# Kernel tuning notes

Measured on AMD Instinct MI355X. Metric: run time of the kernel, lower is better.

The kernel has to match this reference:

```python
import jax, jax.numpy as jnp
import numpy as np

EPS = 1e-5


def gcn_conv(x, src, dst, n_nodes, W, b):
    # x: [B, N, Fin]; src/dst: [E+N] (self loops included); W: [Fout, Fin]
    h = jnp.einsum('bnf,of->bno', x, W)                      # [B, N, Fout]
    deg = jnp.zeros((n_nodes,), h.dtype).at[dst].add(1.0)    # in-degree of A+I
    dinv = jnp.where(deg > 0, 1.0 / jnp.sqrt(deg), 0.0)
    norm = dinv[src] * dinv[dst]                             # [E+N]
    msg = h[:, src, :] * norm[None, :, None]                 # gather along node axis
    out = jnp.zeros_like(h).at[:, dst, :].add(msg)           # scatter-add aggregate
    return out + b


def batchnorm_nodes(x, gamma, beta):
    # torch BatchNorm1d(N) on [B, N, C]: channel axis is N, stats over (B, C)
    mean = jnp.mean(x, axis=(0, 2), keepdims=True)
    var = jnp.mean(jnp.square(x - mean), axis=(0, 2), keepdims=True)
    xn = (x - mean) * jax.lax.rsqrt(var + EPS)
    return xn * gamma[None, :, None] + beta[None, :, None]


def setup_inputs() -> dict:
    key = jax.random.key(0)
    ks = jax.random.split(key, 20)
    B, N, FIN, D, OUT, E = 4096, 64, 67, 2048, 2, 512
    s = 0.1
    d = {}
    d['x_fingerprints'] = jax.random.normal(ks[0], (B, D), jnp.float32)
    d['x_node_features'] = jax.random.normal(ks[1], (B, N, FIN), jnp.float32)
    d['edge_list'] = jax.random.randint(ks[2], (2, E), 0, N)
    d['W1'] = jax.random.normal(ks[3], (64, FIN), jnp.float32) * s
    d['b1'] = jax.random.normal(ks[4], (64,), jnp.float32) * s
    d['g1'] = 1.0 + jax.random.normal(ks[5], (N,), jnp.float32) * s
    d['be1'] = jax.random.normal(ks[6], (N,), jnp.float32) * s
    d['W2'] = jax.random.normal(ks[7], (32, 64), jnp.float32) * s
    d['b2'] = jax.random.normal(ks[8], (32,), jnp.float32) * s
    d['g2'] = 1.0 + jax.random.normal(ks[9], (N,), jnp.float32) * s
    d['be2'] = jax.random.normal(ks[10], (N,), jnp.float32) * s
    d['Wl1'] = jax.random.normal(ks[11], (400, D), jnp.float32) * (s / 4)
    d['bl1'] = jax.random.normal(ks[12], (400,), jnp.float32) * s
    d['Wl2'] = jax.random.normal(ks[13], (64, 400), jnp.float32) * s
    d['bl2'] = jax.random.normal(ks[14], (64,), jnp.float32) * s
    d['Wfc'] = jax.random.normal(ks[15], (OUT, 96), jnp.float32) * s
    d['bfc'] = jax.random.normal(ks[16], (OUT,), jnp.float32) * s
    return d


def reference(x_fingerprints, x_node_features, edge_list, W1, b1, g1, be1,
              W2, b2, g2, be2, Wl1, bl1, Wl2, bl2, Wfc, bfc):
    B, N, _ = x_node_features.shape
    loops = jnp.arange(N)
    src = jnp.concatenate([edge_list[0], loops])  # add self loops (GCNConv default)
    dst = jnp.concatenate([edge_list[1], loops])
    g = gcn_conv(x_node_features, src, dst, N, W1, b1)
    g = jax.nn.relu(batchnorm_nodes(g, g1, be1))
    g = gcn_conv(g, src, dst, N, W2, b2)
    g = jax.nn.relu(batchnorm_nodes(g, g2, be2))           # [B, N, 32]
    pooled = jnp.max(g, axis=1)                             # global_max_pool -> [B, 32]
    h = jax.nn.relu(x_fingerprints @ Wl1.T + bl1)
    h = jax.nn.relu(h @ Wl2.T + bl2)                        # [B, 64]
    out = jnp.concatenate([pooled, h], axis=1) @ Wfc.T + bfc
    return out
```

## Files before the change

### kernel.cpp

```cpp
#include <hip/hip_runtime.h>
#include <hip/hip_bf16.h>
#include <math.h>

typedef __bf16 bf16;
typedef __attribute__((ext_vector_type(8))) __bf16 bf16x8;
typedef __attribute__((ext_vector_type(4))) __bf16 bf16x4;
typedef __attribute__((ext_vector_type(4))) float f32x4;

#define EPSBN 1e-5f
#define B_    4096
#define N_    64
#define FIN_  67
#define E_    512
#define NSLOT 128

__global__ __launch_bounds__(256) void k0_prep(const int* __restrict__ edge,
    const float* __restrict__ W1, const float* __restrict__ W2,
    float* __restrict__ partials,
    bf16* __restrict__ an_hi, bf16* __restrict__ an_lo,
    bf16* __restrict__ wpad,
    bf16* __restrict__ w2pad)
{
    int tid = threadIdx.x;
    for (int i = blockIdx.x * 256 + tid; i < NSLOT * 64 * 4; i += gridDim.x * 256)
        partials[i] = 0.f;
    if (blockIdx.x == 1) {
        for (int i = tid; i < 64 * 104; i += 256) {
            int n = i / 104, f = i % 104;
            wpad[i] = (f < FIN_) ? (bf16)W1[n * FIN_ + f] : (bf16)0.f;
        }
        return;
    }
    if (blockIdx.x == 2) {
        for (int i = tid; i < 32 * 72; i += 256) {
            int o = i / 72, f = i % 72;
            w2pad[i] = (f < 64) ? (bf16)W2[o * 64 + f] : (bf16)0.f;
        }
        return;
    }
    if (blockIdx.x != 0) return;

    __shared__ float An[64 * 64];
    __shared__ int ssrc[E_], sdst[E_];
    __shared__ int deg[N_];
    __shared__ float dinv[N_];
    for (int i = tid; i < 64 * 64; i += 256) An[i] = 0.f;
    for (int i = tid; i < E_; i += 256) { ssrc[i] = edge[i]; sdst[i] = edge[E_ + i]; }
    if (tid < N_) deg[tid] = 1;
    __syncthreads();
    for (int i = tid; i < E_; i += 256) atomicAdd(&deg[sdst[i]], 1);
    __syncthreads();
    if (tid < N_) dinv[tid] = rsqrtf((float)deg[tid]);
    __syncthreads();
    for (int i = tid; i < E_; i += 256) {
        int s = ssrc[i], d = sdst[i];
        atomicAdd(&An[d * 64 + s], dinv[s] * dinv[d]);
    }
    if (tid < N_) atomicAdd(&An[tid * 64 + tid], dinv[tid] * dinv[tid]);
    __syncthreads();
    for (int i = tid; i < 64 * 64; i += 256) {
        float v = An[i];
        bf16 h = (bf16)v;
        an_hi[i] = h;
        an_lo[i] = (bf16)(v - (float)h);
    }
}

__global__ __launch_bounds__(256) void k1_gcn1(
    const float* __restrict__ x,
    const float* __restrict__ b1,
    const bf16* __restrict__ an_hi, const bf16* __restrict__ an_lo,
    const bf16* __restrict__ wpad,
    bf16* __restrict__ g1out,
    float* __restrict__ part1)
{
    __shared__ union {
        struct { float xraw[4352]; bf16 wb[64 * 104]; } s0;
        struct { bf16 hhi[64 * 72]; bf16 hlo[64 * 72]; bf16 ost[64 * 72]; } s1;
    } u;
    int tid = threadIdx.x, b = blockIdx.x;
    int w = tid >> 6, lane = tid & 63, q = lane >> 4, r15 = lane & 15;
    int arow = w * 16 + r15;

    const bf16* ahp = an_hi + arow * 64 + q * 8;
    const bf16* alp = an_lo + arow * 64 + q * 8;
    bf16x8 Ah0 = *(const bf16x8*)ahp;
    bf16x8 Ah1 = *(const bf16x8*)(ahp + 32);
    bf16x8 Al0 = *(const bf16x8*)alp;
    bf16x8 Al1 = *(const bf16x8*)(alp + 32);

    const f32x4* xb4 = (const f32x4*)(x + (size_t)b * (N_ * FIN_));
    f32x4* xl4 = (f32x4*)u.s0.xraw;
    for (int i = tid; i < 1072; i += 256) xl4[i] = xb4[i];
    const bf16x8* wg8 = (const bf16x8*)wpad;
    bf16x8* wl8 = (bf16x8*)u.s0.wb;
    for (int i = tid; i < 832; i += 256) wl8[i] = wg8[i];
    __syncthreads();

    f32x4 z4 = {0.f, 0.f, 0.f, 0.f};
    f32x4 acc[4] = {z4, z4, z4, z4};
    const float* xr = u.s0.xraw + arow * FIN_;
#pragma unroll
    for (int kt = 0; kt < 3; ++kt) {
        bf16x8 a;
        int k0 = kt * 32 + q * 8;
#pragma unroll
        for (int j = 0; j < 8; ++j) {
            int k = k0 + j;
            a[j] = (k < FIN_) ? (bf16)xr[k] : (bf16)0.f;
        }
#pragma unroll
        for (int nt = 0; nt < 4; ++nt) {
            bf16x8 bb = *(const bf16x8*)&u.s0.wb[(nt * 16 + r15) * 104 + k0];
            acc[nt] = __builtin_amdgcn_mfma_f32_16x16x32_bf16(a, bb, acc[nt], 0, 0, 0);
        }
    }
    __syncthreads();

    int sbase = w * 16 + q * 4;
#pragma unroll
    for (int nt = 0; nt < 4; ++nt) {
        int c = nt * 16 + r15;
        bf16x4 hi, lo;
#pragma unroll
        for (int r = 0; r < 4; ++r) {
            float v = acc[nt][r];
            bf16 h = (bf16)v;
            hi[r] = h;
            lo[r] = (bf16)(v - (float)h);
        }
        *(bf16x4*)&u.s1.hhi[c * 72 + sbase] = hi;
        *(bf16x4*)&u.s1.hlo[c * 72 + sbase] = lo;
    }
    __syncthreads();

    f32x4 acc2[4] = {z4, z4, z4, z4};
#pragma unroll
    for (int kt = 0; kt < 2; ++kt) {
        bf16x8 Ahk = kt ? Ah1 : Ah0;
        bf16x8 Alk = kt ? Al1 : Al0;
#pragma unroll
        for (int nt = 0; nt < 4; ++nt) {
            int o = (nt * 16 + r15) * 72 + kt * 32 + q * 8;
            bf16x8 Hh = *(const bf16x8*)&u.s1.hhi[o];
            bf16x8 Hl = *(const bf16x8*)&u.s1.hlo[o];
            acc2[nt] = __builtin_amdgcn_mfma_f32_16x16x32_bf16(Ahk, Hh, acc2[nt], 0, 0, 0);
            acc2[nt] = __builtin_amdgcn_mfma_f32_16x16x32_bf16(Ahk, Hl, acc2[nt], 0, 0, 0);
            acc2[nt] = __builtin_amdgcn_mfma_f32_16x16x32_bf16(Alk, Hh, acc2[nt], 0, 0, 0);
        }
    }

    float rs1[4] = {0.f, 0.f, 0.f, 0.f}, rs2[4] = {0.f, 0.f, 0.f, 0.f};
#pragma unroll
    for (int nt = 0; nt < 4; ++nt) {
        int c = nt * 16 + r15;
        float bc = b1[c];
#pragma unroll
        for (int r = 0; r < 4; ++r) {
            float v = acc2[nt][r] + bc;
            rs1[r] += v; rs2[r] += v * v;
            u.s1.ost[(w * 16 + q * 4 + r) * 72 + c] = (bf16)v;
        }
    }
#pragma unroll
    for (int r = 0; r < 4; ++r)
#pragma unroll
        for (int o = 1; o < 16; o <<= 1) {
            rs1[r] += __shfl_xor(rs1[r], o);
            rs2[r] += __shfl_xor(rs2[r], o);
        }
    if (r15 == 0) {
        int slot = b & (NSLOT - 1);
#pragma unroll
        for (int r = 0; r < 4; ++r) {
            int d = w * 16 + q * 4 + r;
            atomicAdd(&part1[(slot * 64 + d) * 2 + 0], rs1[r]);
            atomicAdd(&part1[(slot * 64 + d) * 2 + 1], rs2[r]);
        }
    }
    __syncthreads();
    int n = tid >> 2, oq = tid & 3;
    bf16x8 o0 = *(const bf16x8*)&u.s1.ost[n * 72 + oq * 16];
    bf16x8 o1 = *(const bf16x8*)&u.s1.ost[n * 72 + oq * 16 + 8];
    bf16* gp = g1out + ((size_t)b * 4096 + n * 64 + oq * 16);
    *(bf16x8*)gp = o0;
    *(bf16x8*)(gp + 8) = o1;
}

__global__ __launch_bounds__(64) void k_bnstats(
    const float* __restrict__ part,
    const float* __restrict__ gamma, const float* __restrict__ beta,
    float* __restrict__ scale, float* __restrict__ shift, float inv_count)
{
    int n = blockIdx.x, t = threadIdx.x;
    float s1 = part[(t * 64 + n) * 2] + part[((t + 64) * 64 + n) * 2];
    float s2 = part[(t * 64 + n) * 2 + 1] + part[((t + 64) * 64 + n) * 2 + 1];
#pragma unroll
    for (int o = 32; o > 0; o >>= 1) { s1 += __shfl_down(s1, o); s2 += __shfl_down(s2, o); }
    if (t == 0) {
        float mean = s1 * inv_count;
        float var = s2 * inv_count - mean * mean;
        float sc = gamma[n] * rsqrtf(var + EPSBN);
        scale[n] = sc;
        shift[n] = beta[n] - mean * sc;
    }
}

__global__ __launch_bounds__(256) void k3_gcn2(
    const bf16* __restrict__ g1out,
    const float* __restrict__ b2,
    const float* __restrict__ scale1, const float* __restrict__ shift1,
    const bf16* __restrict__ an_hi, const bf16* __restrict__ an_lo,
    const bf16* __restrict__ w2pad,
    bf16* __restrict__ g2out,
    float* __restrict__ part2)
{
    __shared__ union {
        struct { bf16 graw[4096]; bf16 wb[32 * 72]; } s0;
        struct { bf16 hhi[32 * 72]; bf16 hlo[32 * 72]; bf16 ost[64 * 40]; } s1;
    } u;
    int tid = threadIdx.x, b = blockIdx.x;
    int w = tid >> 6, lane = tid & 63, q = lane >> 4, r15 = lane & 15;
    int arow = w * 16 + r15;

    const bf16* ahp = an_hi + arow * 64 + q * 8;
    const bf16* alp = an_lo + arow * 64 + q * 8;
    bf16x8 Ah0 = *(const bf16x8*)ahp;
    bf16x8 Ah1 = *(const bf16x8*)(ahp + 32);
    bf16x8 Al0 = *(const bf16x8*)alp;
    bf16x8 Al1 = *(const bf16x8*)(alp + 32);
    float sc = scale1[arow], sh = shift1[arow];

    const bf16x8* gg8 = (const bf16x8*)(g1out + (size_t)b * 4096);
    bf16x8* gl8 = (bf16x8*)u.s0.graw;
    for (int i = tid; i < 512; i += 256) gl8[i] = gg8[i];
    const bf16x8* wg8 = (const bf16x8*)w2pad;
    bf16x8* wl8 = (bf16x8*)u.s0.wb;
    for (int i = tid; i < 288; i += 256) wl8[i] = wg8[i];
    __syncthreads();

    f32x4 z4 = {0.f, 0.f, 0.f, 0.f};
    f32x4 acc[2] = {z4, z4};
#pragma unroll
    for (int kt = 0; kt < 2; ++kt) {
        int k0 = kt * 32 + q * 8;
        bf16x8 raw = *(const bf16x8*)&u.s0.graw[arow * 64 + k0];
        bf16x8 a;
#pragma unroll
        for (int j = 0; j < 8; ++j)
            a[j] = (bf16)fmaxf(fmaf(sc, (float)raw[j], sh), 0.f);
#pragma unroll
        for (int nt = 0; nt < 2; ++nt) {
            bf16x8 bb = *(const bf16x8*)&u.s0.wb[(nt * 16 + r15) * 72 + k0];
            acc[nt] = __builtin_amdgcn_mfma_f32_16x16x32_bf16(a, bb, acc[nt], 0, 0, 0);
        }
    }
    __syncthreads();

    int sbase = w * 16 + q * 4;
#pragma unroll
    for (int nt = 0; nt < 2; ++nt) {
        int c = nt * 16 + r15;
        bf16x4 hi, lo;
#pragma unroll
        for (int r = 0; r < 4; ++r) {
            float v = acc[nt][r];
            bf16 h = (bf16)v;
            hi[r] = h;
            lo[r] = (bf16)(v - (float)h);
        }
        *(bf16x4*)&u.s1.hhi[c * 72 + sbase] = hi;
        *(bf16x4*)&u.s1.hlo[c * 72 + sbase] = lo;
    }
    __syncthreads();

    f32x4 acc2[2] = {z4, z4};
#pragma unroll
    for (int kt = 0; kt < 2; ++kt) {
        bf16x8 Ahk = kt ? Ah1 : Ah0;
        bf16x8 Alk = kt ? Al1 : Al0;
#pragma unroll
        for (int nt = 0; nt < 2; ++nt) {
            int o = (nt * 16 + r15) * 72 + kt * 32 + q * 8;
            bf16x8 Hh = *(const bf16x8*)&u.s1.hhi[o];
            bf16x8 Hl = *(const bf16x8*)&u.s1.hlo[o];
            acc2[nt] = __builtin_amdgcn_mfma_f32_16x16x32_bf16(Ahk, Hh, acc2[nt], 0, 0, 0);
            acc2[nt] = __builtin_amdgcn_mfma_f32_16x16x32_bf16(Ahk, Hl, acc2[nt], 0, 0, 0);
            acc2[nt] = __builtin_amdgcn_mfma_f32_16x16x32_bf16(Alk, Hh, acc2[nt], 0, 0, 0);
        }
    }

    float rs1[4] = {0.f, 0.f, 0.f, 0.f}, rs2[4] = {0.f, 0.f, 0.f, 0.f};
#pragma unroll
    for (int nt = 0; nt < 2; ++nt) {
        int c = nt * 16 + r15;
        float bc = b2[c];
#pragma unroll
        for (int r = 0; r < 4; ++r) {
            float v = acc2[nt][r] + bc;
            rs1[r] += v; rs2[r] += v * v;
            u.s1.ost[(w * 16 + q * 4 + r) * 40 + c] = (bf16)v;
        }
    }
#pragma unroll
    for (int r = 0; r < 4; ++r)
#pragma unroll
        for (int o = 1; o < 16; o <<= 1) {
            rs1[r] += __shfl_xor(rs1[r], o);
            rs2[r] += __shfl_xor(rs2[r], o);
        }
    if (r15 == 0) {
        int slot = b & (NSLOT - 1);
#pragma unroll
        for (int r = 0; r < 4; ++r) {
            int d = w * 16 + q * 4 + r;
            atomicAdd(&part2[(slot * 64 + d) * 2 + 0], rs1[r]);
            atomicAdd(&part2[(slot * 64 + d) * 2 + 1], rs2[r]);
        }
    }
    __syncthreads();
    int n = tid >> 2, oq = tid & 3;
    bf16x8 ov = *(const bf16x8*)&u.s1.ost[n * 40 + oq * 8];
    *(bf16x8*)(g2out + ((size_t)b * 2048 + n * 32 + oq * 8)) = ov;
}

__global__ __launch_bounds__(256) void k6_mlp1(
    const float* __restrict__ A,
    const float* __restrict__ Bw,
    float* __restrict__ part)
{
    __shared__ bf16 As[64 * 36];
    __shared__ bf16 Bs[64 * 36];
    int tid = threadIdx.x;
    int m0 = blockIdx.x * 64, n0 = blockIdx.y * 64, ks = blockIdx.z;
    int row = tid >> 2, seg = tid & 3;
    int w = tid >> 6, lane = tid & 63, q = lane >> 4, r15 = lane & 15;
    f32x4 z4 = {0.f, 0.f, 0.f, 0.f};
    f32x4 acc[4] = {z4, z4, z4, z4};
    const float* pA = A + (size_t)(m0 + row) * 2048 + ks * 512 + seg * 8;
    bool bvalid = (n0 + row) < 400;
    const float* pB = Bw + (size_t)(n0 + row) * 2048 + ks * 512 + seg * 8;

    f32x4 a0 = *(const f32x4*)pA;
    f32x4 a1 = *(const f32x4*)(pA + 4);
    f32x4 c0 = z4, c1 = z4;
    if (bvalid) { c0 = *(const f32x4*)pB; c1 = *(const f32x4*)(pB + 4); }

    for (int kt = 0; kt < 16; ++kt) {
        bf16x8 apk, bpk;
        apk[0] = (bf16)a0[0]; apk[1] = (bf16)a0[1]; apk[2] = (bf16)a0[2]; apk[3] = (bf16)a0[3];
        apk[4] = (bf16)a1[0]; apk[5] = (bf16)a1[1]; apk[6] = (bf16)a1[2]; apk[7] = (bf16)a1[3];
        bpk[0] = (bf16)c0[0]; bpk[1] = (bf16)c0[1]; bpk[2] = (bf16)c0[2]; bpk[3] = (bf16)c0[3];
        bpk[4] = (bf16)c1[0]; bpk[5] = (bf16)c1[1]; bpk[6] = (bf16)c1[2]; bpk[7] = (bf16)c1[3];
        __syncthreads();
        *(bf16x8*)&As[row * 36 + seg * 8] = apk;
        *(bf16x8*)&Bs[row * 36 + seg * 8] = bpk;
        __syncthreads();
        if (kt < 15) {
            pA += 32; pB += 32;
            a0 = *(const f32x4*)pA; a1 = *(const f32x4*)(pA + 4);
            if (bvalid) { c0 = *(const f32x4*)pB; c1 = *(const f32x4*)(pB + 4); }
        }
        bf16x8 a = *(const bf16x8*)&As[(w * 16 + r15) * 36 + q * 8];
#pragma unroll
        for (int nt = 0; nt < 4; ++nt) {
            bf16x8 bb = *(const bf16x8*)&Bs[(nt * 16 + r15) * 36 + q * 8];
            acc[nt] = __builtin_amdgcn_mfma_f32_16x16x32_bf16(a, bb, acc[nt], 0, 0, 0);
        }
    }
    float* pp = part + (size_t)ks * 1638400;
#pragma unroll
    for (int nt = 0; nt < 4; ++nt)
#pragma unroll
        for (int r = 0; r < 4; ++r) {
            int mm = m0 + w * 16 + q * 4 + r;
            int nn = n0 + nt * 16 + r15;
            if (nn < 400) pp[(size_t)mm * 400 + nn] = acc[nt][r];
        }
}

__global__ __launch_bounds__(256) void k6_reduce(
    const float* __restrict__ part,
    const float* __restrict__ bias,
    bf16* __restrict__ h1)
{
    int i = blockIdx.x * 256 + threadIdx.x;
    const f32x4* p = (const f32x4*)part;
    f32x4 s0 = p[i], s1v = p[i + 409600], s2v = p[i + 819200], s3v = p[i + 1228800];
    int nn = (i * 4) % 400;
    f32x4 bv = *(const f32x4*)&bias[nn];
    bf16x4 ov;
    ov[0] = (bf16)fmaxf(s0[0] + s1v[0] + s2v[0] + s3v[0] + bv[0], 0.f);
    ov[1] = (bf16)fmaxf(s0[1] + s1v[1] + s2v[1] + s3v[1] + bv[1], 0.f);
    ov[2] = (bf16)fmaxf(s0[2] + s1v[2] + s2v[2] + s3v[2] + bv[2], 0.f);
    ov[3] = (bf16)fmaxf(s0[3] + s1v[3] + s2v[3] + s3v[3] + bv[3], 0.f);
    *(bf16x4*)&h1[i * 4] = ov;
}

__global__ __launch_bounds__(256) void k7_mlp2(
    const bf16* __restrict__ A,
    const float* __restrict__ Bw,
    const float* __restrict__ bias,
    float* __restrict__ Cout)
{
    __shared__ bf16 As[16 * 416];
    int tid = threadIdx.x;
    int m0 = blockIdx.x * 16;
    for (int i = tid; i < 16 * 50; i += 256) {
        int rr = i / 50, cc = (i % 50) * 8;
        *(bf16x8*)&As[rr * 416 + cc] = *(const bf16x8*)(A + (size_t)(m0 + rr) * 400 + cc);
    }
    if (tid < 32) {
        int rr = tid >> 1, cc = 400 + (tid & 1) * 8;
        bf16x8 z;
#pragma unroll
        for (int k = 0; k < 8; ++k) z[k] = (bf16)0.f;
        *(bf16x8*)&As[rr * 416 + cc] = z;
    }
    __syncthreads();

    int w = tid >> 6, lane = tid & 63, q = lane >> 4, r15 = lane & 15;
    f32x4 acc = {0.f, 0.f, 0.f, 0.f};
    const float* pB = Bw + (size_t)(w * 16 + r15) * 400;
#pragma unroll 4
    for (int kt = 0; kt < 13; ++kt) {
        int k0 = kt * 32 + q * 8;
        bf16x8 a = *(const bf16x8*)&As[r15 * 416 + k0];
        bf16x8 bb;
#pragma unroll
        for (int k = 0; k < 8; ++k) bb[k] = (bf16)0.f;
        if (k0 < 400) {
            f32x4 c0 = *(const f32x4*)(pB + k0);
            f32x4 c1 = *(const f32x4*)(pB + k0 + 4);
            bb[0] = (bf16)c0[0]; bb[1] = (bf16)c0[1]; bb[2] = (bf16)c0[2]; bb[3] = (bf16)c0[3];
            bb[4] = (bf16)c1[0]; bb[5] = (bf16)c1[1]; bb[6] = (bf16)c1[2]; bb[7] = (bf16)c1[3];
        }
        acc = __builtin_amdgcn_mfma_f32_16x16x32_bf16(a, bb, acc, 0, 0, 0);
    }
#pragma unroll
    for (int r = 0; r < 4; ++r) {
        int mm = m0 + q * 4 + r;
        int nn = w * 16 + r15;
        float v = fmaxf(acc[r] + bias[nn], 0.f);
        Cout[(size_t)mm * 64 + nn] = v;
    }
}

__global__ __launch_bounds__(256) void k8_final(
    const bf16* __restrict__ g2out,
    const float* __restrict__ scale2, const float* __restrict__ shift2,
    const float* __restrict__ h2,
    const float* __restrict__ Wfc,
    const float* __restrict__ bfc,
    float* __restrict__ out)
{
    __shared__ float s2s[64], sh2s[64];
    int tid = threadIdx.x;
    if (tid < 64) { s2s[tid] = scale2[tid]; sh2s[tid] = shift2[tid]; }
    __syncthreads();
    int w = tid >> 6, lane = tid & 63;
    int b = blockIdx.x * 4 + w;
    int c = lane & 31, half = lane >> 5;
    const bf16* gb = g2out + (size_t)b * 2048;
    float mx = 0.f;
    for (int i = 0; i < 32; ++i) {
        int n = half * 32 + i;
        float v = (float)gb[n * 32 + c];
        float val = fmaf(s2s[n], v, sh2s[n]);
        mx = fmaxf(mx, val);
    }
    mx = fmaxf(mx, __shfl_xor(mx, 32));
    float h2v = h2[(size_t)b * 64 + lane];
#pragma unroll
    for (int o = 0; o < 2; ++o) {
        float t = h2v * Wfc[o * 96 + 32 + lane];
        if (half == 0) t += mx * Wfc[o * 96 + c];
#pragma unroll
        for (int off = 32; off > 0; off >>= 1) t += __shfl_xor(t, off);
        if (lane == 0) out[(size_t)b * 2 + o] = t + bfc[o];
    }
}

extern "C" void kernel_launch(void* const* d_in, const int* in_sizes, int n_in,
                              void* d_out, int out_size, void* d_ws, size_t ws_size,
                              hipStream_t stream)
{
    const float* x_fp   = (const float*)d_in[0];
    const float* x_node = (const float*)d_in[1];
    const int*   edge   = (const int*)d_in[2];
    const float* W1     = (const float*)d_in[3];
    const float* b1     = (const float*)d_in[4];
    const float* g1     = (const float*)d_in[5];
    const float* be1    = (const float*)d_in[6];
    const float* W2     = (const float*)d_in[7];
    const float* b2     = (const float*)d_in[8];
    const float* g2     = (const float*)d_in[9];
    const float* be2    = (const float*)d_in[10];
    const float* Wl1    = (const float*)d_in[11];
    const float* bl1    = (const float*)d_in[12];
    const float* Wl2    = (const float*)d_in[13];
    const float* bl2    = (const float*)d_in[14];
    const float* Wfc    = (const float*)d_in[15];
    const float* bfc    = (const float*)d_in[16];
    float* out = (float*)d_out;

    char* ws = (char*)d_ws;
    float* scale1  = (float*)(ws + 5632);
    float* shift1  = (float*)(ws + 5888);
    float* scale2  = (float*)(ws + 6144);
    float* shift2  = (float*)(ws + 6400);
    float* part1   = (float*)(ws + 8192);
    float* part2   = (float*)(ws + 8192 + 65536);
    bf16*  g1out   = (bf16*)(ws + 139264);
    float* part6   = (float*)(ws + 139264);
    bf16*  g2out   = (bf16*)(ws + 33693696ull);
    bf16*  h1      = (bf16*)(ws + 50470912ull);
    float* h2      = (float*)(ws + 53747712ull);
    bf16*  an_hi   = (bf16*)(ws + 53747712ull);
    bf16*  an_lo   = (bf16*)(ws + 53747712ull + 8192);
    bf16*  wpad    = (bf16*)(ws + 53747712ull + 16384);
    bf16*  w2pad   = (bf16*)(ws + 53747712ull + 32768);

    k0_prep<<<dim3(64), dim3(256), 0, stream>>>(edge, W1, W2, part1, an_hi, an_lo, wpad, w2pad);
    k1_gcn1<<<dim3(4096), dim3(256), 0, stream>>>(x_node, b1, an_hi, an_lo, wpad, g1out, part1);
    k_bnstats<<<dim3(64), dim3(64), 0, stream>>>(part1, g1, be1, scale1, shift1,
                                                 1.f / (4096.f * 64.f));
    k3_gcn2<<<dim3(4096), dim3(256), 0, stream>>>(g1out, b2, scale1, shift1,
                                                  an_hi, an_lo, w2pad, g2out, part2);
    k_bnstats<<<dim3(64), dim3(64), 0, stream>>>(part2, g2, be2, scale2, shift2,
                                                 1.f / (4096.f * 32.f));
    k6_mlp1<<<dim3(64, 7, 4), dim3(256), 0, stream>>>(x_fp, Wl1, part6);
    k6_reduce<<<dim3(1600), dim3(256), 0, stream>>>(part6, bl1, h1);
    k7_mlp2<<<dim3(256), dim3(256), 0, stream>>>(h1, Wl2, bl2, h2);
    k8_final<<<dim3(1024), dim3(256), 0, stream>>>(g2out, scale2, shift2, h2, Wfc, bfc, out);
}
```

Before: 269.0 us.

## Process four graphs per block with register prefetch and register-resident weights

Both GCN kernels now loop over four batch elements per block. Each block keeps its W fragments and bias in registers instead of staging them through shared memory, and loads the next graph's input into registers while the current one is computed. BN partial statistics are now taken from the bf16-rounded outputs after the store, with a short 4-lane shuffle. Launch bounds are tightened to raise occupancy. In exchange the grid is 4x smaller, there are more registers per thread, and the statistics are computed on rounded values.

Result: faster. 241.3 us (-10.3%).

```diff
diff --git a/kernel.cpp b/kernel.cpp
--- a/kernel.cpp
+++ b/kernel.cpp
@@ -66,7 +66,7 @@
     }
 }
 
-__global__ __launch_bounds__(256) void k1_gcn1(
+__global__ __launch_bounds__(256, 3) void k1_gcn1(
     const float* __restrict__ x,
     const float* __restrict__ b1,
     const bf16* __restrict__ an_hi, const bf16* __restrict__ an_lo,
@@ -74,13 +74,21 @@
     bf16* __restrict__ g1out,
     float* __restrict__ part1)
 {
-    __shared__ union {
-        struct { float xraw[4352]; bf16 wb[64 * 104]; } s0;
-        struct { bf16 hhi[64 * 72]; bf16 hlo[64 * 72]; bf16 ost[64 * 72]; } s1;
-    } u;
-    int tid = threadIdx.x, b = blockIdx.x;
+    __shared__ float xraw[4352];
+    __shared__ bf16 hhi[64 * 72];
+    __shared__ bf16 hlo[64 * 72];
+    __shared__ bf16 ost[64 * 72];
+
+    int tid = threadIdx.x;
     int w = tid >> 6, lane = tid & 63, q = lane >> 4, r15 = lane & 15;
     int arow = w * 16 + r15;
+
+    bf16x8 wf[3][4];
+#pragma unroll
+    for (int kt = 0; kt < 3; ++kt)
+#pragma unroll
+        for (int nt = 0; nt < 4; ++nt)
+            wf[kt][nt] = *(const bf16x8*)&wpad[(nt * 16 + r15) * 104 + kt * 32 + q * 8];
 
     const bf16* ahp = an_hi + arow * 64 + q * 8;
     const bf16* alp = an_lo + arow * 64 + q * 8;
@@ -89,102 +97,112 @@
     bf16x8 Al0 = *(const bf16x8*)alp;
     bf16x8 Al1 = *(const bf16x8*)(alp + 32);
 
-    const f32x4* xb4 = (const f32x4*)(x + (size_t)b * (N_ * FIN_));
-    f32x4* xl4 = (f32x4*)u.s0.xraw;
-    for (int i = tid; i < 1072; i += 256) xl4[i] = xb4[i];
-    const bf16x8* wg8 = (const bf16x8*)wpad;
-    bf16x8* wl8 = (bf16x8*)u.s0.wb;
-    for (int i = tid; i < 832; i += 256) wl8[i] = wg8[i];
-    __syncthreads();
-
+    float bc[4];
+#pragma unroll
+    for (int nt = 0; nt < 4; ++nt) bc[nt] = b1[nt * 16 + r15];
+
+    size_t b0 = (size_t)blockIdx.x * 4;
+    const f32x4* xb4 = (const f32x4*)(x + b0 * 4288);
+
+    f32x4 pre0 = xb4[tid], pre1 = xb4[tid + 256], pre2 = xb4[tid + 512], pre3 = xb4[tid + 768];
+    f32x4 pre4 = {0.f, 0.f, 0.f, 0.f};
+    if (tid < 48) pre4 = xb4[tid + 1024];
+
+    f32x4* xl4 = (f32x4*)xraw;
     f32x4 z4 = {0.f, 0.f, 0.f, 0.f};
-    f32x4 acc[4] = {z4, z4, z4, z4};
-    const float* xr = u.s0.xraw + arow * FIN_;
-#pragma unroll
-    for (int kt = 0; kt < 3; ++kt) {
-        bf16x8 a;
-        int k0 = kt * 32 + q * 8;
+
+#pragma unroll 1
+    for (int g = 0; g < 4; ++g) {
+        int b = (int)b0 + g;
+        xl4[tid] = pre0; xl4[tid + 256] = pre1; xl4[tid + 512] = pre2; xl4[tid + 768] = pre3;
+        if (tid < 48) xl4[tid + 1024] = pre4;
+        __syncthreads();
+
+        f32x4 acc[4] = {z4, z4, z4, z4};
+        const float* xr = xraw + arow * FIN_;
+#pragma unroll
+        for (int kt = 0; kt < 3; ++kt) {
+            bf16x8 a;
+            if (kt < 2) {
+                int k0 = kt * 32 + q * 8;
+#pragma unroll
+                for (int j = 0; j < 8; ++j) a[j] = (bf16)xr[k0 + j];
+            } else {
+#pragma unroll
+                for (int j = 0; j < 8; ++j) a[j] = (bf16)0.f;
+                if (q == 0) { a[0] = (bf16)xr[64]; a[1] = (bf16)xr[65]; a[2] = (bf16)xr[66]; }
+            }
+#pragma unroll
+            for (int nt = 0; nt < 4; ++nt)
+                acc[nt] = __builtin_amdgcn_mfma_f32_16x16x32_bf16(a, wf[kt][nt], acc[nt], 0, 0, 0);
+        }
+        if (g < 3) {
+            const f32x4* xn = xb4 + (size_t)(g + 1) * 1072;
+            pre0 = xn[tid]; pre1 = xn[tid + 256]; pre2 = xn[tid + 512]; pre3 = xn[tid + 768];
+            if (tid < 48) pre4 = xn[tid + 1024];
+        }
+        __syncthreads();
+
+        int sbase = w * 16 + q * 4;
+#pragma unroll
+        for (int nt = 0; nt < 4; ++nt) {
+            int c = nt * 16 + r15;
+            bf16x4 hi, lo;
+#pragma unroll
+            for (int r = 0; r < 4; ++r) {
+                float v = acc[nt][r];
+                bf16 h = (bf16)v;
+                hi[r] = h; lo[r] = (bf16)(v - (float)h);
+            }
+            *(bf16x4*)&hhi[c * 72 + sbase] = hi;
+            *(bf16x4*)&hlo[c * 72 + sbase] = lo;
+        }
+        __syncthreads();
+
+        f32x4 acc2[4] = {z4, z4, z4, z4};
+#pragma unroll
+        for (int kt = 0; kt < 2; ++kt) {
+            bf16x8 Ahk = kt ? Ah1 : Ah0;
+            bf16x8 Alk = kt ? Al1 : Al0;
+#pragma unroll
+            for (int nt = 0; nt < 4; ++nt) {
+                int o = (nt * 16 + r15) * 72 + kt * 32 + q * 8;
+                bf16x8 Hh = *(const bf16x8*)&hhi[o];
+                bf16x8 Hl = *(const bf16x8*)&hlo[o];
+                acc2[nt] = __builtin_amdgcn_mfma_f32_16x16x32_bf16(Ahk, Hh, acc2[nt], 0, 0, 0);
+                acc2[nt] = __builtin_amdgcn_mfma_f32_16x16x32_bf16(Ahk, Hl, acc2[nt], 0, 0, 0);
+                acc2[nt] = __builtin_amdgcn_mfma_f32_16x16x32_bf16(Alk, Hh, acc2[nt], 0, 0, 0);
+            }
+        }
+#pragma unroll
+        for (int nt = 0; nt < 4; ++nt) {
+            int c = nt * 16 + r15;
+#pragma unroll
+            for (int r = 0; r < 4; ++r)
+                ost[(sbase + r) * 72 + c] = (bf16)(acc2[nt][r] + bc[nt]);
+        }
+        __syncthreads();
+
+        int n = tid >> 2, oq = tid & 3;
+        bf16x8 o0 = *(const bf16x8*)&ost[n * 72 + oq * 16];
+        bf16x8 o1 = *(const bf16x8*)&ost[n * 72 + oq * 16 + 8];
+        bf16* gp = g1out + ((size_t)b * 4096 + n * 64 + oq * 16);
+        *(bf16x8*)gp = o0;
+        *(bf16x8*)(gp + 8) = o1;
+        float s1 = 0.f, s2 = 0.f;
 #pragma unroll
         for (int j = 0; j < 8; ++j) {
-            int k = k0 + j;
-            a[j] = (k < FIN_) ? (bf16)xr[k] : (bf16)0.f;
-        }
-#pragma unroll
-        for (int nt = 0; nt < 4; ++nt) {
-            bf16x8 bb = *(const bf16x8*)&u.s0.wb[(nt * 16 + r15) * 104 + k0];
-            acc[nt] = __builtin_amdgcn_mfma_f32_16x16x32_bf16(a, bb, acc[nt], 0, 0, 0);
-        }
-    }
-    __syncthreads();
-
-    int sbase = w * 16 + q * 4;
-#pragma unroll
-    for (int nt = 0; nt < 4; ++nt) {
-        int c = nt * 16 + r15;
-        bf16x4 hi, lo;
-#pragma unroll
-        for (int r = 0; r < 4; ++r) {
-            float v = acc[nt][r];
-            bf16 h = (bf16)v;
-            hi[r] = h;
-            lo[r] = (bf16)(v - (float)h);
-        }
-        *(bf16x4*)&u.s1.hhi[c * 72 + sbase] = hi;
-        *(bf16x4*)&u.s1.hlo[c * 72 + sbase] = lo;
-    }
-    __syncthreads();
-
-    f32x4 acc2[4] = {z4, z4, z4, z4};
-#pragma unroll
-    for (int kt = 0; kt < 2; ++kt) {
-        bf16x8 Ahk = kt ? Ah1 : Ah0;
-        bf16x8 Alk = kt ? Al1 : Al0;
-#pragma unroll
-        for (int nt = 0; nt < 4; ++nt) {
-            int o = (nt * 16 + r15) * 72 + kt * 32 + q * 8;
-            bf16x8 Hh = *(const bf16x8*)&u.s1.hhi[o];
-            bf16x8 Hl = *(const bf16x8*)&u.s1.hlo[o];
-            acc2[nt] = __builtin_amdgcn_mfma_f32_16x16x32_bf16(Ahk, Hh, acc2[nt], 0, 0, 0);
-            acc2[nt] = __builtin_amdgcn_mfma_f32_16x16x32_bf16(Ahk, Hl, acc2[nt], 0, 0, 0);
-            acc2[nt] = __builtin_amdgcn_mfma_f32_16x16x32_bf16(Alk, Hh, acc2[nt], 0, 0, 0);
-        }
-    }
-
-    float rs1[4] = {0.f, 0.f, 0.f, 0.f}, rs2[4] = {0.f, 0.f, 0.f, 0.f};
-#pragma unroll
-    for (int nt = 0; nt < 4; ++nt) {
-        int c = nt * 16 + r15;
-        float bc = b1[c];
-#pragma unroll
-        for (int r = 0; r < 4; ++r) {
-            float v = acc2[nt][r] + bc;
-            rs1[r] += v; rs2[r] += v * v;
-            u.s1.ost[(w * 16 + q * 4 + r) * 72 + c] = (bf16)v;
-        }
-    }
-#pragma unroll
-    for (int r = 0; r < 4; ++r)
-#pragma unroll
-        for (int o = 1; o < 16; o <<= 1) {
-            rs1[r] += __shfl_xor(rs1[r], o);
-            rs2[r] += __shfl_xor(rs2[r], o);
-        }
-    if (r15 == 0) {
-        int slot = b & (NSLOT - 1);
-#pragma unroll
-        for (int r = 0; r < 4; ++r) {
-            int d = w * 16 + q * 4 + r;
-            atomicAdd(&part1[(slot * 64 + d) * 2 + 0], rs1[r]);
-            atomicAdd(&part1[(slot * 64 + d) * 2 + 1], rs2[r]);
-        }
-    }
-    __syncthreads();
-    int n = tid >> 2, oq = tid & 3;
-    bf16x8 o0 = *(const bf16x8*)&u.s1.ost[n * 72 + oq * 16];
-    bf16x8 o1 = *(const bf16x8*)&u.s1.ost[n * 72 + oq * 16 + 8];
-    bf16* gp = g1out + ((size_t)b * 4096 + n * 64 + oq * 16);
-    *(bf16x8*)gp = o0;
-    *(bf16x8*)(gp + 8) = o1;
+            float v0 = (float)o0[j], v1 = (float)o1[j];
+            s1 += v0 + v1; s2 += v0 * v0 + v1 * v1;
+        }
+        s1 += __shfl_xor(s1, 1); s1 += __shfl_xor(s1, 2);
+        s2 += __shfl_xor(s2, 1); s2 += __shfl_xor(s2, 2);
+        if (oq == 0) {
+            int slot = b & (NSLOT - 1);
+            atomicAdd(&part1[(slot * 64 + n) * 2 + 0], s1);
+            atomicAdd(&part1[(slot * 64 + n) * 2 + 1], s2);
+        }
+    }
 }
 
 __global__ __launch_bounds__(64) void k_bnstats(
@@ -206,7 +224,7 @@
     }
 }
 
-__global__ __launch_bounds__(256) void k3_gcn2(
+__global__ __launch_bounds__(256, 4) void k3_gcn2(
     const bf16* __restrict__ g1out,
     const float* __restrict__ b2,
     const float* __restrict__ scale1, const float* __restrict__ shift1,
@@ -215,13 +233,21 @@
     bf16* __restrict__ g2out,
     float* __restrict__ part2)
 {
-    __shared__ union {
-        struct { bf16 graw[4096]; bf16 wb[32 * 72]; } s0;
-        struct { bf16 hhi[32 * 72]; bf16 hlo[32 * 72]; bf16 ost[64 * 40]; } s1;
-    } u;
-    int tid = threadIdx.x, b = blockIdx.x;
+    __shared__ bf16 ya[64 * 72];
+    __shared__ bf16 hhi[32 * 72];
+    __shared__ bf16 hlo[32 * 72];
+    __shared__ bf16 ost[64 * 40];
+
+    int tid = threadIdx.x;
     int w = tid >> 6, lane = tid & 63, q = lane >> 4, r15 = lane & 15;
     int arow = w * 16 + r15;
+
+    bf16x8 wf[2][2];
+#pragma unroll
+    for (int kt = 0; kt < 2; ++kt)
+#pragma unroll
+        for (int nt = 0; nt < 2; ++nt)
+            wf[kt][nt] = *(const bf16x8*)&w2pad[(nt * 16 + r15) * 72 + kt * 32 + q * 8];
 
     const bf16* ahp = an_hi + arow * 64 + q * 8;
     const bf16* alp = an_lo + arow * 64 + q * 8;
@@ -230,98 +256,98 @@
     bf16x8 Al0 = *(const bf16x8*)alp;
     bf16x8 Al1 = *(const bf16x8*)(alp + 32);
     float sc = scale1[arow], sh = shift1[arow];
-
-    const bf16x8* gg8 = (const bf16x8*)(g1out + (size_t)b * 4096);
-    bf16x8* gl8 = (bf16x8*)u.s0.graw;
-    for (int i = tid; i < 512; i += 256) gl8[i] = gg8[i];
-    const bf16x8* wg8 = (const bf16x8*)w2pad;
-    bf16x8* wl8 = (bf16x8*)u.s0.wb;
-    for (int i = tid; i < 288; i += 256) wl8[i] = wg8[i];
-    __syncthreads();
-
+    float bc[2] = { b2[r15], b2[16 + r15] };
+
+    size_t b0 = (size_t)blockIdx.x * 4;
+    const bf16x8* gg8 = (const bf16x8*)(g1out + b0 * 4096);
+    bf16x8 p0 = gg8[tid], p1 = gg8[tid + 256];
+
+    int r0 = tid >> 3, c0 = (tid & 7) * 8;
     f32x4 z4 = {0.f, 0.f, 0.f, 0.f};
-    f32x4 acc[2] = {z4, z4};
-#pragma unroll
-    for (int kt = 0; kt < 2; ++kt) {
-        int k0 = kt * 32 + q * 8;
-        bf16x8 raw = *(const bf16x8*)&u.s0.graw[arow * 64 + k0];
-        bf16x8 a;
-#pragma unroll
-        for (int j = 0; j < 8; ++j)
-            a[j] = (bf16)fmaxf(fmaf(sc, (float)raw[j], sh), 0.f);
+
+#pragma unroll 1
+    for (int g = 0; g < 4; ++g) {
+        int b = (int)b0 + g;
+        *(bf16x8*)&ya[r0 * 72 + c0] = p0;
+        *(bf16x8*)&ya[(r0 + 32) * 72 + c0] = p1;
+        __syncthreads();
+
+        f32x4 acc[2] = {z4, z4};
+#pragma unroll
+        for (int kt = 0; kt < 2; ++kt) {
+            int k0 = kt * 32 + q * 8;
+            bf16x8 raw = *(const bf16x8*)&ya[arow * 72 + k0];
+            bf16x8 a;
+#pragma unroll
+            for (int j = 0; j < 8; ++j)
+                a[j] = (bf16)fmaxf(fmaf(sc, (float)raw[j], sh), 0.f);
+#pragma unroll
+            for (int nt = 0; nt < 2; ++nt)
+                acc[nt] = __builtin_amdgcn_mfma_f32_16x16x32_bf16(a, wf[kt][nt], acc[nt], 0, 0, 0);
+        }
+        if (g < 3) {
+            p0 = gg8[(size_t)(g + 1) * 512 + tid];
+            p1 = gg8[(size_t)(g + 1) * 512 + tid + 256];
+        }
+        __syncthreads();
+
+        int sbase = w * 16 + q * 4;
 #pragma unroll
         for (int nt = 0; nt < 2; ++nt) {
-            bf16x8 bb = *(const bf16x8*)&u.s0.wb[(nt * 16 + r15) * 72 + k0];
-            acc[nt] = __builtin_amdgcn_mfma_f32_16x16x32_bf16(a, bb, acc[nt], 0, 0, 0);
-        }
-    }
-    __syncthreads();
-
-    int sbase = w * 16 + q * 4;
-#pragma unroll
-    for (int nt = 0; nt < 2; ++nt) {
-        int c = nt * 16 + r15;
-        bf16x4 hi, lo;
-#pragma unroll
-        for (int r = 0; r < 4; ++r) {
-            float v = acc[nt][r];
-            bf16 h = (bf16)v;
-            hi[r] = h;
-            lo[r] = (bf16)(v - (float)h);
-        }
-        *(bf16x4*)&u.s1.hhi[c * 72 + sbase] = hi;
-        *(bf16x4*)&u.s1.hlo[c * 72 + sbase] = lo;
-    }
-    __syncthreads();
-
-    f32x4 acc2[2] = {z4, z4};
-#pragma unroll
-    for (int kt = 0; kt < 2; ++kt) {
-        bf16x8 Ahk = kt ? Ah1 : Ah0;
-        bf16x8 Alk = kt ? Al1 : Al0;
+            int c = nt * 16 + r15;
+            bf16x4 hi, lo;
+#pragma unroll
+            for (int r = 0; r < 4; ++r) {
+                float v = acc[nt][r];
+                bf16 h = (bf16)v;
+                hi[r] = h; lo[r] = (bf16)(v - (float)h);
+            }
+            *(bf16x4*)&hhi[c * 72 + sbase] = hi;
+            *(bf16x4*)&hlo[c * 72 + sbase] = lo;
+        }
+        __syncthreads();
+
+        f32x4 acc2[2] = {z4, z4};
+#pragma unroll
+        for (int kt = 0; kt < 2; ++kt) {
+            bf16x8 Ahk = kt ? Ah1 : Ah0;
+            bf16x8 Alk = kt ? Al1 : Al0;
+#pragma unroll
+            for (int nt = 0; nt < 2; ++nt) {
+                int o = (nt * 16 + r15) * 72 + kt * 32 + q * 8;
+                bf16x8 Hh = *(const bf16x8*)&hhi[o];
+                bf16x8 Hl = *(const bf16x8*)&hlo[o];
+                acc2[nt] = __builtin_amdgcn_mfma_f32_16x16x32_bf16(Ahk, Hh, acc2[nt], 0, 0, 0);
+                acc2[nt] = __builtin_amdgcn_mfma_f32_16x16x32_bf16(Ahk, Hl, acc2[nt], 0, 0, 0);
+                acc2[nt] = __builtin_amdgcn_mfma_f32_16x16x32_bf16(Alk, Hh, acc2[nt], 0, 0, 0);
+            }
+        }
 #pragma unroll
         for (int nt = 0; nt < 2; ++nt) {
-            int o = (nt * 16 + r15) * 72 + kt * 32 + q * 8;
-            bf16x8 Hh = *(const bf16x8*)&u.s1.hhi[o];
-            bf16x8 Hl = *(const bf16x8*)&u.s1.hlo[o];
-            acc2[nt] = __builtin_amdgcn_mfma_f32_16x16x32_bf16(Ahk, Hh, acc2[nt], 0, 0, 0);
-            acc2[nt] = __builtin_amdgcn_mfma_f32_16x16x32_bf16(Ahk, Hl, acc2[nt], 0, 0, 0);
-            acc2[nt] = __builtin_amdgcn_mfma_f32_16x16x32_bf16(Alk, Hh, acc2[nt], 0, 0, 0);
-        }
-    }
-
-    float rs1[4] = {0.f, 0.f, 0.f, 0.f}, rs2[4] = {0.f, 0.f, 0.f, 0.f};
-#pragma unroll
-    for (int nt = 0; nt < 2; ++nt) {
-        int c = nt * 16 + r15;
-        float bc = b2[c];
-#pragma unroll
-        for (int r = 0; r < 4; ++r) {
-            float v = acc2[nt][r] + bc;
-            rs1[r] += v; rs2[r] += v * v;
-            u.s1.ost[(w * 16 + q * 4 + r) * 40 + c] = (bf16)v;
-        }
-    }
-#pragma unroll
-    for (int r = 0; r < 4; ++r)
-#pragma unroll
-        for (int o = 1; o < 16; o <<= 1) {
-            rs1[r] += __shfl_xor(rs1[r], o);
-            rs2[r] += __shfl_xor(rs2[r], o);
-        }
-    if (r15 == 0) {
-        int slot = b & (NSLOT - 1);
-#pragma unroll
-        for (int r = 0; r < 4; ++r) {
-            int d = w * 16 + q * 4 + r;
-            atomicAdd(&part2[(slot * 64 + d) * 2 + 0], rs1[r]);
-            atomicAdd(&part2[(slot * 64 + d) * 2 + 1], rs2[r]);
-        }
-    }
-    __syncthreads();
-    int n = tid >> 2, oq = tid & 3;
-    bf16x8 ov = *(const bf16x8*)&u.s1.ost[n * 40 + oq * 8];
-    *(bf16x8*)(g2out + ((size_t)b * 2048 + n * 32 + oq * 8)) = ov;
+            int c = nt * 16 + r15;
+#pragma unroll
+            for (int r = 0; r < 4; ++r)
+                ost[(sbase + r) * 40 + c] = (bf16)(acc2[nt][r] + bc[nt]);
+        }
+        __syncthreads();
+
+        int n = tid >> 2, oq = tid & 3;
+        bf16x8 ov = *(const bf16x8*)&ost[n * 40 + oq * 8];
+        *(bf16x8*)(g2out + ((size_t)b * 2048 + n * 32 + oq * 8)) = ov;
+        float s1 = 0.f, s2 = 0.f;
+#pragma unroll
+        for (int j = 0; j < 8; ++j) {
+            float v = (float)ov[j];
+            s1 += v; s2 += v * v;
+        }
+        s1 += __shfl_xor(s1, 1); s1 += __shfl_xor(s1, 2);
+        s2 += __shfl_xor(s2, 1); s2 += __shfl_xor(s2, 2);
+        if (oq == 0) {
+            int slot = b & (NSLOT - 1);
+            atomicAdd(&part2[(slot * 64 + n) * 2 + 0], s1);
+            atomicAdd(&part2[(slot * 64 + n) * 2 + 1], s2);
+        }
+    }
 }
 
 __global__ __launch_bounds__(256) void k6_mlp1(
@@ -522,10 +548,10 @@
     bf16*  w2pad   = (bf16*)(ws + 53747712ull + 32768);
 
     k0_prep<<<dim3(64), dim3(256), 0, stream>>>(edge, W1, W2, part1, an_hi, an_lo, wpad, w2pad);
-    k1_gcn1<<<dim3(4096), dim3(256), 0, stream>>>(x_node, b1, an_hi, an_lo, wpad, g1out, part1);
+    k1_gcn1<<<dim3(1024), dim3(256), 0, stream>>>(x_node, b1, an_hi, an_lo, wpad, g1out, part1);
     k_bnstats<<<dim3(64), dim3(64), 0, stream>>>(part1, g1, be1, scale1, shift1,
                                                  1.f / (4096.f * 64.f));
-    k3_gcn2<<<dim3(4096), dim3(256), 0, stream>>>(g1out, b2, scale1, shift1,
+    k3_gcn2<<<dim3(1024), dim3(256), 0, stream>>>(g1out, b2, scale1, shift1,
                                                   an_hi, an_lo, w2pad, g2out, part2);
     k_bnstats<<<dim3(64), dim3(64), 0, stream>>>(part2, g2, be2, scale2, shift2,
                                                  1.f / (4096.f * 32.f));
```
